# Kernel tuning notes

Measured on AMD Instinct MI355X. Metric: run time of the kernel, lower is better.

Reference implementation:

```python
import jax, jax.numpy as jnp
import numpy as np

B, S, FIN, FM = 4, 1024, 3, 5
L, D, H, FF, OUT = 4, 256, 8, 1024, 20
DH = D // H
LN_EPS = 1e-5


def setup_inputs() -> dict:
    key = jax.random.key(0)
    ks = jax.random.split(key, 12)
    g = lambda k, sh: (jax.random.normal(k, sh, dtype=jnp.float32) * 0.02)
    return {
        'input_coord': jax.random.normal(ks[0], (B, S, FIN), dtype=jnp.float32),
        'input_for_mask': jax.random.normal(ks[1], (B, S, FM), dtype=jnp.float32),
        'padding_mask': jax.random.randint(ks[2], (B, S), 0, 2).astype(bool),
        'w_in': g(ks[3], (D, FIN)), 'b_in': jnp.zeros((D,), jnp.float32),
        'w_qkv': g(ks[4], (L, 3 * D, D)), 'b_qkv': jnp.zeros((L, 3 * D), jnp.float32),
        'w_o': g(ks[5], (L, D, D)), 'b_o': jnp.zeros((L, D), jnp.float32),
        'w_ff1': g(ks[6], (L, FF, D)), 'b_ff1': jnp.zeros((L, FF), jnp.float32),
        'w_ff2': g(ks[7], (L, D, FF)), 'b_ff2': jnp.zeros((L, D), jnp.float32),
        'ln1_g': jnp.ones((L, D), jnp.float32), 'ln1_b': jnp.zeros((L, D), jnp.float32),
        'ln2_g': jnp.ones((L, D), jnp.float32), 'ln2_b': jnp.zeros((L, D), jnp.float32),
        'w_dec': g(ks[8], (OUT, D)), 'b_dec': jnp.zeros((OUT,), jnp.float32),
    }


def _layer_norm(x, g, b):
    m = jnp.mean(x, axis=-1, keepdims=True)
    v = jnp.mean((x - m) ** 2, axis=-1, keepdims=True)
    return (x - m) * jax.lax.rsqrt(v + LN_EPS) * g + b


def _distance_mask(points, padding_mask,
                   z_0_limit=197.4, phi_r_ratio_limit=0.001825, angular_separation_limit=1.797):
    # True = pair is MASKED OUT (torch bool attn_mask semantics)
    points = jax.lax.stop_gradient(points)
    big = jnp.asarray(1e6, points.dtype)
    n = points.shape[1]
    pad2 = padding_mask[:, None, :] | padding_mask[:, :, None]
    pad2 = pad2 | jnp.eye(n, dtype=bool)[None]  # diagonal filled True in torch code
    npm = ~pad2  # non-padding (and off-diagonal) pairs
    col = lambda i: (points[..., i][:, :, None], points[..., i][:, None, :])  # (point1, point2)
    z1, z2 = col(0); r1, r2 = col(1); p1, p2 = col(2); e1, e2 = col(3)
    r_diff = jnp.where(npm, r2 - r1, big)
    z_0 = jnp.where((r_diff != 0) & npm, jnp.abs(z1 - r1 * (z2 - z1) / r_diff), big)
    phi_diff = jnp.where(npm, jnp.abs(p2 - p1), big)
    phi_diff = jnp.where((phi_diff > np.pi) & npm, 2.0 * np.pi - phi_diff, phi_diff)
    phi_r_ratio = jnp.where(npm, phi_diff / (jnp.abs(r_diff) + 1e-8), big)
    ang_sep = jnp.where(npm, jnp.sqrt((e2 - e1) ** 2 + phi_diff ** 2), big)
    return npm & (z_0 > z_0_limit) & (phi_r_ratio > phi_r_ratio_limit) & (ang_sep > angular_separation_limit)


def reference(input_coord, input_for_mask, padding_mask,
              w_in, b_in, w_qkv, b_qkv, w_o, b_o,
              w_ff1, b_ff1, w_ff2, b_ff2,
              ln1_g, ln1_b, ln2_g, ln2_b, w_dec, b_dec):
    b, s, _ = input_coord.shape
    x = input_coord @ w_in.T + b_in  # [B,S,D]
    dmask = _distance_mask(input_for_mask, padding_mask)
    # torch merges bool attn_mask with key_padding_mask (padded keys blocked)
    blocked = dmask | padding_mask[:, None, :]  # [B,S,S], True = blocked
    neg = jnp.asarray(-1e9, x.dtype)
    scale = 1.0 / np.sqrt(DH)
    for l in range(w_qkv.shape[0]):
        qkv = x @ w_qkv[l].T + b_qkv[l]
        q, k, v = jnp.split(qkv, 3, axis=-1)
        to_heads = lambda t: t.reshape(b, s, H, DH).transpose(0, 2, 1, 3)  # [B,H,S,dh]
        q, k, v = to_heads(q), to_heads(k), to_heads(v)
        scores = jnp.einsum('bhqd,bhkd->bhqk', q, k) * scale
        scores = jnp.where(blocked[:, None], neg, scores)
        attn = jax.nn.softmax(scores, axis=-1)
        o = jnp.einsum('bhqk,bhkd->bhqd', attn, v)
        o = o.transpose(0, 2, 1, 3).reshape(b, s, -1) @ w_o[l].T + b_o[l]
        x = _layer_norm(x + o, ln1_g[l], ln1_b[l])  # post-norm encoder layer
        h = jax.nn.relu(x @ w_ff1[l].T + b_ff1[l]) @ w_ff2[l].T + b_ff2[l]
        x = _layer_norm(x + h, ln2_g[l], ln2_b[l])
    return x @ w_dec.T + b_dec  # [B,S,OUT]
```

## Files before the change

### kernel.cpp

```cpp
#include <hip/hip_runtime.h>
#include <math.h>

#define BATCH 4
#define SEQ   1024
#define DM    256
#define NH    8
#define DHD   32
#define NL    4
#define FF1   1024
#define OUTD  20

typedef _Float16 f16;
typedef _Float16 f16x8 __attribute__((ext_vector_type(8)));
typedef _Float16 f16x4 __attribute__((ext_vector_type(4)));
typedef float    f32x4 __attribute__((ext_vector_type(4)));

__global__ void pad_kernel(const void* __restrict__ praw, unsigned char* __restrict__ pad)
{
    __shared__ int isInt;
    const int tid = threadIdx.x;
    const unsigned char* pb = (const unsigned char*)praw;
    if (tid == 0) isInt = 1;
    __syncthreads();
    unsigned char any = 0;
    for (int p = tid; p < BATCH * SEQ; p += 1024)
        if ((p & 3) && pb[p]) any = 1;
    if (any) isInt = 0;
    __syncthreads();
    const int ii = isInt;
    for (int e = tid; e < BATCH * SEQ; e += 1024)
        pad[e] = ii ? (unsigned char)(((const int*)praw)[e] != 0)
                    : (unsigned char)(pb[e] != 0);
}

__global__ __launch_bounds__(256) void mask_kernel(const float* __restrict__ P,
                                                   const unsigned char* __restrict__ pad,
                                                   unsigned int* __restrict__ mbits)
{
    const int bi = blockIdx.x;
    const int b = bi >> 10, i = bi & 1023;
    const float* Pb = P + (size_t)b * SEQ * 5;
    const float z1 = Pb[i * 5 + 0], r1 = Pb[i * 5 + 1];
    const float p1 = Pb[i * 5 + 2], e1 = Pb[i * 5 + 3];
    const unsigned char pad_i = pad[bi];
    unsigned int* mrow = mbits + (size_t)bi * (SEQ / 32);
    const float PI_F  = 3.14159265358979323846f;
    const float TPI_F = 6.28318530717958647692f;
    const int lane = threadIdx.x & 63;
    const int wv = threadIdx.x >> 6;
    for (int t = 0; t < 4; ++t) {
        const int j = threadIdx.x + t * 256;
        const unsigned char pad_j = pad[b * SEQ + j];
        bool blocked;
        if (pad_i || pad_j || i == j) {
            blocked = (pad_j != 0);
        } else {
            const float z2 = Pb[j * 5 + 0], r2 = Pb[j * 5 + 1];
            const float p2 = Pb[j * 5 + 2], e2 = Pb[j * 5 + 3];
            const float rdiff = r2 - r1;
            const float z0 = (rdiff != 0.f) ? fabsf(z1 - r1 * (z2 - z1) / rdiff) : 1e6f;
            float pdiff = fabsf(p2 - p1);
            if (pdiff > PI_F) pdiff = TPI_F - pdiff;
            const float ratio = pdiff / (fabsf(rdiff) + 1e-8f);
            const float ang = sqrtf((e2 - e1) * (e2 - e1) + pdiff * pdiff);
            blocked = (z0 > 197.4f) && (ratio > 0.001825f) && (ang > 1.797f);
        }
        const unsigned long long bal = __ballot(blocked);
        if (lane == 0) {
            const int w0 = wv * 2 + t * 8;
            mrow[w0 + 0] = (unsigned int)bal;
            mrow[w0 + 1] = (unsigned int)(bal >> 32);
        }
    }
}

__global__ __launch_bounds__(256) void embed_kernel(const float* __restrict__ in,
                                                    const float* __restrict__ w_in,
                                                    const float* __restrict__ b_in,
                                                    float* __restrict__ x,
                                                    f16* __restrict__ xh)
{
    const int row = blockIdx.x;
    const int d = threadIdx.x;
    const float i0 = in[row * 3 + 0], i1 = in[row * 3 + 1], i2 = in[row * 3 + 2];
    const float v = b_in[d] + i0 * w_in[d * 3 + 0] + i1 * w_in[d * 3 + 1] + i2 * w_in[d * 3 + 2];
    x[(size_t)row * DM + d] = v;
    xh[(size_t)row * DM + d] = (f16)v;
}

__global__ __launch_bounds__(256) void castw_kernel(const float* __restrict__ src,
                                                    f16* __restrict__ dst, int n)
{
    const int i = (blockIdx.x * 256 + threadIdx.x) * 8;
    if (i >= n) return;
    f16x8 o;
    #pragma unroll
    for (int j = 0; j < 8; ++j) o[j] = (f16)src[i + j];
    *(f16x8*)&dst[i] = o;
}

template<int BT>
__global__ __launch_bounds__(256) void mgemm_kernel(const f16* __restrict__ A,
                                                    const f16* __restrict__ W,
                                                    const float* __restrict__ bias,
                                                    void* __restrict__ C,
                                                    int M, int N, int K, int relu, int of16)
{
    constexpr int WT = BT / 2;
    constexpr int MF = WT / 16;
    constexpr int LDT = 40;
    __shared__ f16 Al[BT * LDT];
    __shared__ f16 Wl[BT * LDT];
    const int tid = threadIdx.x;
    const int lane = tid & 63, g = lane >> 4, fr = lane & 15;
    const int wv = tid >> 6, wm = wv >> 1, wn = wv & 1;
    const int m0 = blockIdx.y * BT, n0 = blockIdx.x * BT;

    f32x4 acc[MF][MF] = {};
    for (int k0 = 0; k0 < K; k0 += 32) {
        __syncthreads();
        #pragma unroll
        for (int u = 0; u < BT / 64; ++u) {
            const int row = (tid >> 2) + u * 64, col = (tid & 3) * 8;
            *(f16x8*)&Al[row * LDT + col] = *(const f16x8*)&A[(size_t)(m0 + row) * K + k0 + col];
            *(f16x8*)&Wl[row * LDT + col] = *(const f16x8*)&W[(size_t)(n0 + row) * K + k0 + col];
        }
        __syncthreads();
        f16x8 af[MF], wf[MF];
        #pragma unroll
        for (int m = 0; m < MF; ++m)
            af[m] = *(const f16x8*)&Al[(wm * WT + m * 16 + fr) * LDT + g * 8];
        #pragma unroll
        for (int n = 0; n < MF; ++n)
            wf[n] = *(const f16x8*)&Wl[(wn * WT + n * 16 + fr) * LDT + g * 8];
        #pragma unroll
        for (int m = 0; m < MF; ++m)
            #pragma unroll
            for (int n = 0; n < MF; ++n)
                acc[m][n] = __builtin_amdgcn_mfma_f32_16x16x32_f16(af[m], wf[n], acc[m][n], 0, 0, 0);
    }
    #pragma unroll
    for (int m = 0; m < MF; ++m)
        #pragma unroll
        for (int n = 0; n < MF; ++n) {
            const int col = n0 + wn * WT + n * 16 + fr;
            const float bs = bias[col];
            #pragma unroll
            for (int r = 0; r < 4; ++r) {
                const int row = m0 + wm * WT + m * 16 + g * 4 + r;
                float v = acc[m][n][r] + bs;
                if (relu) v = fmaxf(v, 0.f);
                if (of16) ((f16*)C)[(size_t)row * N + col] = (f16)v;
                else      ((float*)C)[(size_t)row * N + col] = v;
            }
        }
}

__global__ __launch_bounds__(256) void split_heads_kernel(const f16* __restrict__ qkv,
                                                          f16* __restrict__ Qh,
                                                          f16* __restrict__ Kh,
                                                          f16* __restrict__ Vh)
{
    const int row = blockIdx.x;
    const int b = row >> 10, s = row & 1023;
    const int c = threadIdx.x;
    const int h = c >> 5, d = c & 31;
    const size_t dst = (((size_t)(b * NH + h) * SEQ) + s) * DHD + d;
    const f16* src = qkv + (size_t)row * 768;
    Qh[dst] = src[c];
    Kh[dst] = src[256 + c];
    Vh[dst] = src[512 + c];
}

__global__ __launch_bounds__(256) void attn3_kernel(const f16* __restrict__ Qh,
                                                    const f16* __restrict__ Kh,
                                                    const f16* __restrict__ Vh,
                                                    const unsigned int* __restrict__ mbits,
                                                    f16* __restrict__ out)
{
    __shared__ f16 Kl[64 * 40];
    __shared__ f16 Vt[32 * 72];
    __shared__ f16 Ql[64 * 40];
    __shared__ f16 Pl[4][16 * 72];
    __shared__ unsigned int Ml[64][2];
    const int bh = blockIdx.y, b = bh >> 3, h = bh & 7;
    const int q0 = blockIdx.x * 64;
    const int tid = threadIdx.x, wv = tid >> 6, lane = tid & 63;
    const int g = lane >> 4, fr = lane & 15;
    const size_t kvbase = (size_t)bh * SEQ * DHD;

    {
        const int row = tid >> 2, col = (tid & 3) * 8;
        *(f16x8*)&Ql[row * 40 + col] = *(const f16x8*)&Qh[kvbase + (size_t)(q0 + row) * DHD + col];
    }
    const int mrowbase = b * SEQ + q0;
    const float scale = 0.17677669529663687f;
    float mrun = -3.0e38f, lrun = 0.f;
    f32x4 o0 = {0.f, 0.f, 0.f, 0.f}, o1 = {0.f, 0.f, 0.f, 0.f};

    for (int t = 0; t < 16; ++t) {
        __syncthreads();
        {
            const int row = tid >> 2, col = (tid & 3) * 8;
            *(f16x8*)&Kl[row * 40 + col] = *(const f16x8*)&Kh[kvbase + (size_t)(t * 64 + row) * DHD + col];
        }
        {
            const int k = tid & 63, d0 = (tid >> 6) * 8;
            const f16x8 v = *(const f16x8*)&Vh[kvbase + (size_t)(t * 64 + k) * DHD + d0];
            #pragma unroll
            for (int j = 0; j < 8; ++j) Vt[(d0 + j) * 72 + k] = v[j];
        }
        if (tid < 128) {
            const int i = tid >> 1, w = tid & 1;
            Ml[i][w] = mbits[(size_t)(mrowbase + i) * (SEQ / 32) + t * 2 + w];
        }
        __syncthreads();

        const f16x8 bq = *(const f16x8*)&Ql[(wv * 16 + fr) * 40 + g * 8];
        f32x4 s[4];
        #pragma unroll
        for (int f = 0; f < 4; ++f) {
            const f16x8 ak = *(const f16x8*)&Kl[(f * 16 + fr) * 40 + g * 8];
            const f32x4 z = {0.f, 0.f, 0.f, 0.f};
            s[f] = __builtin_amdgcn_mfma_f32_16x16x32_f16(ak, bq, z, 0, 0, 0);
        }
        const unsigned long long mb =
            ((unsigned long long)Ml[wv * 16 + fr][1] << 32) | (unsigned long long)Ml[wv * 16 + fr][0];
        float tm = -3.0e38f;
        #pragma unroll
        for (int f = 0; f < 4; ++f)
            #pragma unroll
            for (int r = 0; r < 4; ++r) {
                const int kk = f * 16 + g * 4 + r;
                const float v = ((mb >> kk) & 1ULL) ? -1e9f : s[f][r] * scale;
                s[f][r] = v;
                tm = fmaxf(tm, v);
            }
        tm = fmaxf(tm, __shfl_xor(tm, 16, 64));
        tm = fmaxf(tm, __shfl_xor(tm, 32, 64));
        const float mnew = fmaxf(mrun, tm);
        const float resc = __expf(mrun - mnew);
        mrun = mnew;
        lrun *= resc;
        float ps = 0.f;
        #pragma unroll
        for (int f = 0; f < 4; ++f)
            #pragma unroll
            for (int r = 0; r < 4; ++r) {
                const float p = __expf(s[f][r] - mnew);
                s[f][r] = p;
                ps += p;
            }
        ps += __shfl_xor(ps, 16, 64);
        ps += __shfl_xor(ps, 32, 64);
        lrun += ps;
        #pragma unroll
        for (int r = 0; r < 4; ++r) {
            const float rs = __shfl(resc, g * 4 + r, 64);
            o0[r] *= rs;
            o1[r] *= rs;
        }
        #pragma unroll
        for (int f = 0; f < 4; ++f) {
            f16x4 pw = { (f16)s[f][0], (f16)s[f][1], (f16)s[f][2], (f16)s[f][3] };
            *(f16x4*)&Pl[wv][fr * 72 + f * 16 + g * 4] = pw;
        }
        #pragma unroll
        for (int kh = 0; kh < 2; ++kh) {
            const f16x8 pa = *(const f16x8*)&Pl[wv][fr * 72 + kh * 32 + g * 8];
            const f16x8 v0 = *(const f16x8*)&Vt[fr * 72 + kh * 32 + g * 8];
            const f16x8 v1 = *(const f16x8*)&Vt[(16 + fr) * 72 + kh * 32 + g * 8];
            o0 = __builtin_amdgcn_mfma_f32_16x16x32_f16(pa, v0, o0, 0, 0, 0);
            o1 = __builtin_amdgcn_mfma_f32_16x16x32_f16(pa, v1, o1, 0, 0, 0);
        }
    }
    #pragma unroll
    for (int r = 0; r < 4; ++r) {
        const float inv = 1.f / __shfl(lrun, g * 4 + r, 64);
        const int qg = q0 + wv * 16 + g * 4 + r;
        f16* orow = out + ((size_t)(b * SEQ + qg)) * DM + h * DHD;
        orow[fr]      = (f16)(o0[r] * inv);
        orow[16 + fr] = (f16)(o1[r] * inv);
    }
}

__global__ __launch_bounds__(256) void add_ln_kernel(float* __restrict__ x,
                                                     f16* __restrict__ xh,
                                                     const float* __restrict__ t,
                                                     const float* __restrict__ g,
                                                     const float* __restrict__ b)
{
    __shared__ float red[256];
    const int row = blockIdx.x, tid = threadIdx.x;
    const size_t idx = (size_t)row * DM + tid;
    const float v = x[idx] + t[idx];
    red[tid] = v;
    __syncthreads();
    for (int s = 128; s; s >>= 1) { if (tid < s) red[tid] += red[tid + s]; __syncthreads(); }
    const float mean = red[0] * (1.f / DM);
    __syncthreads();
    const float d = v - mean;
    red[tid] = d * d;
    __syncthreads();
    for (int s = 128; s; s >>= 1) { if (tid < s) red[tid] += red[tid + s]; __syncthreads(); }
    const float var = red[0] * (1.f / DM);
    const float rs = rsqrtf(var + 1e-5f);
    const float o = d * rs * g[tid] + b[tid];
    x[idx] = o;
    xh[idx] = (f16)o;
}

__global__ __launch_bounds__(256) void dec_kernel(const float* __restrict__ x,
                                                  const float* __restrict__ w,
                                                  const float* __restrict__ bias,
                                                  float* __restrict__ out)
{
    const int idx = blockIdx.x * 256 + threadIdx.x;
    if (idx >= BATCH * SEQ * OUTD) return;
    const int row = idx / OUTD, o = idx % OUTD;
    const float* xr = x + (size_t)row * DM;
    const float* wr = w + o * DM;
    float s = bias[o];
    for (int d = 0; d < DM; ++d) s += xr[d] * wr[d];
    out[idx] = s;
}

extern "C" void kernel_launch(void* const* d_in, const int* in_sizes, int n_in,
                              void* d_out, int out_size, void* d_ws, size_t ws_size,
                              hipStream_t stream)
{
    (void)in_sizes; (void)n_in; (void)out_size; (void)ws_size;
    const float* in_coord = (const float*)d_in[0];
    const float* in_maskf = (const float*)d_in[1];
    const void*  praw     = d_in[2];
    const float* w_in  = (const float*)d_in[3];
    const float* b_in  = (const float*)d_in[4];
    const float* w_qkv = (const float*)d_in[5];
    const float* b_qkv = (const float*)d_in[6];
    const float* w_o   = (const float*)d_in[7];
    const float* b_o   = (const float*)d_in[8];
    const float* w_ff1 = (const float*)d_in[9];
    const float* b_ff1 = (const float*)d_in[10];
    const float* w_ff2 = (const float*)d_in[11];
    const float* b_ff2 = (const float*)d_in[12];
    const float* ln1_g = (const float*)d_in[13];
    const float* ln1_b = (const float*)d_in[14];
    const float* ln2_g = (const float*)d_in[15];
    const float* ln2_b = (const float*)d_in[16];
    const float* w_dec = (const float*)d_in[17];
    const float* b_dec = (const float*)d_in[18];

    const int ROWS = BATCH * SEQ;
    float* x   = (float*)d_ws;
    float* tmp = x + 1048576;
    f16* us = (f16*)(tmp + 1048576);
    f16* xh    = us;  us += 1048576;
    f16* qkvb  = us;  us += 3145728;
    f16* Qh    = us;  us += 1048576;
    f16* Kh    = us;  us += 1048576;
    f16* Vh    = us;  us += 1048576;
    f16* attno = us;  us += 1048576;
    f16* hb    = us;  us += 4194304;
    f16* wqb   = us;  us += 786432;
    f16* wob   = us;  us += 262144;
    f16* w1b   = us;  us += 1048576;
    f16* w2b   = us;  us += 1048576;
    unsigned int*  mbits  = (unsigned int*)us;
    unsigned char* padb   = (unsigned char*)(mbits + 131072);

    hipLaunchKernelGGL(pad_kernel, dim3(1), dim3(1024), 0, stream, praw, padb);
    hipLaunchKernelGGL(mask_kernel, dim3(BATCH * SEQ), dim3(256), 0, stream,
                       in_maskf, padb, mbits);
    hipLaunchKernelGGL(embed_kernel, dim3(ROWS), dim3(256), 0, stream,
                       in_coord, w_in, b_in, x, xh);
    hipLaunchKernelGGL(castw_kernel, dim3(786432 / 2048), dim3(256), 0, stream, w_qkv, wqb, 786432);
    hipLaunchKernelGGL(castw_kernel, dim3(262144 / 2048), dim3(256), 0, stream, w_o,  wob, 262144);
    hipLaunchKernelGGL(castw_kernel, dim3(1048576 / 2048), dim3(256), 0, stream, w_ff1, w1b, 1048576);
    hipLaunchKernelGGL(castw_kernel, dim3(1048576 / 2048), dim3(256), 0, stream, w_ff2, w2b, 1048576);

    for (int l = 0; l < NL; ++l) {
        hipLaunchKernelGGL((mgemm_kernel<128>), dim3(768 / 128, ROWS / 128), dim3(256), 0, stream,
                           xh, wqb + (size_t)l * 196608, b_qkv + l * 768, (void*)qkvb,
                           ROWS, 768, 256, 0, 1);
        hipLaunchKernelGGL(split_heads_kernel, dim3(ROWS), dim3(256), 0, stream,
                           qkvb, Qh, Kh, Vh);
        hipLaunchKernelGGL(attn3_kernel, dim3(SEQ / 64, BATCH * NH), dim3(256), 0, stream,
                           Qh, Kh, Vh, mbits, attno);
        hipLaunchKernelGGL((mgemm_kernel<64>), dim3(256 / 64, ROWS / 64), dim3(256), 0, stream,
                           attno, wob + (size_t)l * 65536, b_o + l * 256, (void*)tmp,
                           ROWS, 256, 256, 0, 0);
        hipLaunchKernelGGL(add_ln_kernel, dim3(ROWS), dim3(256), 0, stream,
                           x, xh, tmp, ln1_g + l * DM, ln1_b + l * DM);
        hipLaunchKernelGGL((mgemm_kernel<128>), dim3(1024 / 128, ROWS / 128), dim3(256), 0, stream,
                           xh, w1b + (size_t)l * 262144, b_ff1 + l * 1024, (void*)hb,
                           ROWS, 1024, 256, 1, 1);
        hipLaunchKernelGGL((mgemm_kernel<64>), dim3(256 / 64, ROWS / 64), dim3(256), 0, stream,
                           hb, w2b + (size_t)l * 262144, b_ff2 + l * 256, (void*)tmp,
                           ROWS, 256, 1024, 0, 0);
        hipLaunchKernelGGL(add_ln_kernel, dim3(ROWS), dim3(256), 0, stream,
                           x, xh, tmp, ln2_g + l * DM, ln2_b + l * DM);
    }

    hipLaunchKernelGGL(dec_kernel, dim3((ROWS * OUTD + 255) / 256), dim3(256), 0, stream,
                       x, w_dec, b_dec, (float*)d_out);
}
```

Baseline: 487.1 us.

## Fuse head split into QKV GEMM, widen K step, merge weight casts

The QKV GEMM now writes Q, K and V straight into per-head layout, which removes the separate split_heads kernel and the staging qkv buffer. The GEMM K-tile grows from 32 to 64, with two MFMA sub-steps per shared-memory load, so there are half as many barriers. All GEMMs now use 64-wide tiles to launch more blocks, and the four weight-cast launches become one kernel. The scattered per-head stores in the epilogue may coalesce less well, and smaller tiles give less data reuse per block.

```diff
diff --git a/kernel.cpp b/kernel.cpp
--- a/kernel.cpp
+++ b/kernel.cpp
@@ -88,15 +88,23 @@
     xh[(size_t)row * DM + d] = (f16)v;
 }
 
-__global__ __launch_bounds__(256) void castw_kernel(const float* __restrict__ src,
-                                                    f16* __restrict__ dst, int n)
+__global__ __launch_bounds__(256) void castw4_kernel(const float* __restrict__ s0, f16* __restrict__ d0, int n0,
+                                                     const float* __restrict__ s1, f16* __restrict__ d1, int n1,
+                                                     const float* __restrict__ s2, f16* __restrict__ d2, int n2,
+                                                     const float* __restrict__ s3, f16* __restrict__ d3, int n3)
 {
     const int i = (blockIdx.x * 256 + threadIdx.x) * 8;
-    if (i >= n) return;
+    const float* s; f16* d; int base;
+    if      (i < n0)                { s = s0; d = d0; base = 0; }
+    else if (i < n0 + n1)           { s = s1; d = d1; base = n0; }
+    else if (i < n0 + n1 + n2)      { s = s2; d = d2; base = n0 + n1; }
+    else if (i < n0 + n1 + n2 + n3) { s = s3; d = d3; base = n0 + n1 + n2; }
+    else return;
+    const int j = i - base;
     f16x8 o;
     #pragma unroll
-    for (int j = 0; j < 8; ++j) o[j] = (f16)src[i + j];
-    *(f16x8*)&dst[i] = o;
+    for (int k = 0; k < 8; ++k) o[k] = (f16)s[j + k];
+    *(f16x8*)&d[j] = o;
 }
 
 template<int BT>
@@ -104,11 +112,14 @@
                                                     const f16* __restrict__ W,
                                                     const float* __restrict__ bias,
                                                     void* __restrict__ C,
-                                                    int M, int N, int K, int relu, int of16)
+                                                    int M, int N, int K, int relu, int mode,
+                                                    f16* __restrict__ Qh,
+                                                    f16* __restrict__ Kh,
+                                                    f16* __restrict__ Vh)
 {
     constexpr int WT = BT / 2;
     constexpr int MF = WT / 16;
-    constexpr int LDT = 40;
+    constexpr int LDT = 72;
     __shared__ f16 Al[BT * LDT];
     __shared__ f16 Wl[BT * LDT];
     const int tid = threadIdx.x;
@@ -117,27 +128,31 @@
     const int m0 = blockIdx.y * BT, n0 = blockIdx.x * BT;
 
     f32x4 acc[MF][MF] = {};
-    for (int k0 = 0; k0 < K; k0 += 32) {
+    for (int k0 = 0; k0 < K; k0 += 64) {
         __syncthreads();
         #pragma unroll
-        for (int u = 0; u < BT / 64; ++u) {
-            const int row = (tid >> 2) + u * 64, col = (tid & 3) * 8;
+        for (int u = 0; u < BT / 32; ++u) {
+            const int idx = tid + u * 256;
+            const int row = idx >> 3, col = (idx & 7) * 8;
             *(f16x8*)&Al[row * LDT + col] = *(const f16x8*)&A[(size_t)(m0 + row) * K + k0 + col];
             *(f16x8*)&Wl[row * LDT + col] = *(const f16x8*)&W[(size_t)(n0 + row) * K + k0 + col];
         }
         __syncthreads();
-        f16x8 af[MF], wf[MF];
-        #pragma unroll
-        for (int m = 0; m < MF; ++m)
-            af[m] = *(const f16x8*)&Al[(wm * WT + m * 16 + fr) * LDT + g * 8];
-        #pragma unroll
-        for (int n = 0; n < MF; ++n)
-            wf[n] = *(const f16x8*)&Wl[(wn * WT + n * 16 + fr) * LDT + g * 8];
-        #pragma unroll
-        for (int m = 0; m < MF; ++m)
+        #pragma unroll
+        for (int ks = 0; ks < 2; ++ks) {
+            f16x8 af[MF], wf[MF];
+            #pragma unroll
+            for (int m = 0; m < MF; ++m)
+                af[m] = *(const f16x8*)&Al[(wm * WT + m * 16 + fr) * LDT + ks * 32 + g * 8];
             #pragma unroll
             for (int n = 0; n < MF; ++n)
-                acc[m][n] = __builtin_amdgcn_mfma_f32_16x16x32_f16(af[m], wf[n], acc[m][n], 0, 0, 0);
+                wf[n] = *(const f16x8*)&Wl[(wn * WT + n * 16 + fr) * LDT + ks * 32 + g * 8];
+            #pragma unroll
+            for (int m = 0; m < MF; ++m)
+                #pragma unroll
+                for (int n = 0; n < MF; ++n)
+                    acc[m][n] = __builtin_amdgcn_mfma_f32_16x16x32_f16(af[m], wf[n], acc[m][n], 0, 0, 0);
+        }
     }
     #pragma unroll
     for (int m = 0; m < MF; ++m)
@@ -150,26 +165,20 @@
                 const int row = m0 + wm * WT + m * 16 + g * 4 + r;
                 float v = acc[m][n][r] + bs;
                 if (relu) v = fmaxf(v, 0.f);
-                if (of16) ((f16*)C)[(size_t)row * N + col] = (f16)v;
-                else      ((float*)C)[(size_t)row * N + col] = v;
+                if (mode == 0) {
+                    ((float*)C)[(size_t)row * N + col] = v;
+                } else if (mode == 1) {
+                    ((f16*)C)[(size_t)row * N + col] = (f16)v;
+                } else {
+                    const int b = row >> 10, s = row & 1023;
+                    const int sec = col >> 8, c = col & 255;
+                    const int h = c >> 5, d = c & 31;
+                    const size_t dst = (((size_t)(b * NH + h) * SEQ) + s) * DHD + d;
+                    f16* base = (sec == 0) ? Qh : (sec == 1) ? Kh : Vh;
+                    base[dst] = (f16)v;
+                }
             }
         }
-}
-
-__global__ __launch_bounds__(256) void split_heads_kernel(const f16* __restrict__ qkv,
-                                                          f16* __restrict__ Qh,
-                                                          f16* __restrict__ Kh,
-                                                          f16* __restrict__ Vh)
-{
-    const int row = blockIdx.x;
-    const int b = row >> 10, s = row & 1023;
-    const int c = threadIdx.x;
-    const int h = c >> 5, d = c & 31;
-    const size_t dst = (((size_t)(b * NH + h) * SEQ) + s) * DHD + d;
-    const f16* src = qkv + (size_t)row * 768;
-    Qh[dst] = src[c];
-    Kh[dst] = src[256 + c];
-    Vh[dst] = src[512 + c];
 }
 
 __global__ __launch_bounds__(256) void attn3_kernel(const f16* __restrict__ Qh,
@@ -355,7 +364,6 @@
     float* tmp = x + 1048576;
     f16* us = (f16*)(tmp + 1048576);
     f16* xh    = us;  us += 1048576;
-    f16* qkvb  = us;  us += 3145728;
     f16* Qh    = us;  us += 1048576;
     f16* Kh    = us;  us += 1048576;
     f16* Vh    = us;  us += 1048576;
@@ -373,30 +381,29 @@
                        in_maskf, padb, mbits);
     hipLaunchKernelGGL(embed_kernel, dim3(ROWS), dim3(256), 0, stream,
                        in_coord, w_in, b_in, x, xh);
-    hipLaunchKernelGGL(castw_kernel, dim3(786432 / 2048), dim3(256), 0, stream, w_qkv, wqb, 786432);
-    hipLaunchKernelGGL(castw_kernel, dim3(262144 / 2048), dim3(256), 0, stream, w_o,  wob, 262144);
-    hipLaunchKernelGGL(castw_kernel, dim3(1048576 / 2048), dim3(256), 0, stream, w_ff1, w1b, 1048576);
-    hipLaunchKernelGGL(castw_kernel, dim3(1048576 / 2048), dim3(256), 0, stream, w_ff2, w2b, 1048576);
+    hipLaunchKernelGGL(castw4_kernel, dim3(1536), dim3(256), 0, stream,
+                       w_qkv, wqb, 786432,
+                       w_o,   wob, 262144,
+                       w_ff1, w1b, 1048576,
+                       w_ff2, w2b, 1048576);
 
     for (int l = 0; l < NL; ++l) {
-        hipLaunchKernelGGL((mgemm_kernel<128>), dim3(768 / 128, ROWS / 128), dim3(256), 0, stream,
-                           xh, wqb + (size_t)l * 196608, b_qkv + l * 768, (void*)qkvb,
-                           ROWS, 768, 256, 0, 1);
-        hipLaunchKernelGGL(split_heads_kernel, dim3(ROWS), dim3(256), 0, stream,
-                           qkvb, Qh, Kh, Vh);
+        hipLaunchKernelGGL((mgemm_kernel<64>), dim3(768 / 64, ROWS / 64), dim3(256), 0, stream,
+                           xh, wqb + (size_t)l * 196608, b_qkv + l * 768, (void*)0,
+                           ROWS, 768, 256, 0, 2, Qh, Kh, Vh);
         hipLaunchKernelGGL(attn3_kernel, dim3(SEQ / 64, BATCH * NH), dim3(256), 0, stream,
                            Qh, Kh, Vh, mbits, attno);
         hipLaunchKernelGGL((mgemm_kernel<64>), dim3(256 / 64, ROWS / 64), dim3(256), 0, stream,
                            attno, wob + (size_t)l * 65536, b_o + l * 256, (void*)tmp,
-                           ROWS, 256, 256, 0, 0);
+                           ROWS, 256, 256, 0, 0, (f16*)0, (f16*)0, (f16*)0);
         hipLaunchKernelGGL(add_ln_kernel, dim3(ROWS), dim3(256), 0, stream,
                            x, xh, tmp, ln1_g + l * DM, ln1_b + l * DM);
-        hipLaunchKernelGGL((mgemm_kernel<128>), dim3(1024 / 128, ROWS / 128), dim3(256), 0, stream,
+        hipLaunchKernelGGL((mgemm_kernel<64>), dim3(1024 / 64, ROWS / 64), dim3(256), 0, stream,
                            xh, w1b + (size_t)l * 262144, b_ff1 + l * 1024, (void*)hb,
-                           ROWS, 1024, 256, 1, 1);
+                           ROWS, 1024, 256, 1, 1, (f16*)0, (f16*)0, (f16*)0);
         hipLaunchKernelGGL((mgemm_kernel<64>), dim3(256 / 64, ROWS / 64), dim3(256), 0, stream,
                            hb, w2b + (size_t)l * 262144, b_ff2 + l * 256, (void*)tmp,
-                           ROWS, 256, 1024, 0, 0);
+                           ROWS, 256, 1024, 0, 0, (f16*)0, (f16*)0, (f16*)0);
         hipLaunchKernelGGL(add_ln_kernel, dim3(ROWS), dim3(256), 0, stream,
                            x, xh, tmp, ln2_g + l * DM, ln2_b + l * DM);
     }
```

New measurement: 509.2 us. +4.5%, slower.
